# Kernel tuning notes

Measured on AMD Instinct MI355X. Metric: run time of the kernel, lower is better.

## Reference

```python
import jax, jax.numpy as jnp
import numpy as np

L, H, F_IN, OUT = 6, 2048, 2048, 2048
LN_EPS = 1e-5


def setup_inputs() -> dict:
    key = jax.random.key(0)
    ks = jax.random.split(key, 10)
    bound = 1.0 / np.sqrt(H)
    u = lambda k, shape: jax.random.uniform(k, shape, jnp.float32, -bound, bound)
    return {
        "x": jax.random.normal(ks[0], (1, 1, F_IN), jnp.float32),
        "hidden": jax.random.normal(ks[1], (L, 1, H), jnp.float32),
        "w_ih": u(ks[2], (L, 3 * H, H)),   # layer0 input size == H by construction
        "w_hh": u(ks[3], (L, 3 * H, H)),
        "b_ih": u(ks[4], (L, 3 * H)),
        "b_hh": u(ks[5], (L, 3 * H)),
        "ln_gamma": jnp.ones((H,), jnp.float32),
        "ln_beta": jnp.zeros((H,), jnp.float32),
        "lin_w": u(ks[6], (OUT, H)),
        "lin_b": u(ks[7], (OUT,)),
    }


def _gru_stack(x_t, hidden, w_ih, w_hh, b_ih, b_hh):
    # x_t: [B, H]; hidden: [L, B, H]. PyTorch gate order: r, z, n.
    def layer(inp, params):
        wi, wh, bi, bh, h = params
        gi = (inp @ wi.T + bi).reshape(inp.shape[0], 3, -1)  # [B,3,H]
        gh = (h @ wh.T + bh).reshape(h.shape[0], 3, -1)
        r = jax.nn.sigmoid(gi[:, 0] + gh[:, 0])
        z = jax.nn.sigmoid(gi[:, 1] + gh[:, 1])
        n = jnp.tanh(gi[:, 2] + r * gh[:, 2])
        h_new = (1.0 - z) * n + z * h
        return h_new, h_new

    top, new_hidden = jax.lax.scan(layer, x_t, (w_ih, w_hh, b_ih, b_hh, hidden))
    return top, new_hidden  # [B,H], [L,B,H]


def reference(x, hidden, w_ih, w_hh, b_ih, b_hh, ln_gamma, ln_beta, lin_w, lin_b):
    x_t = x[:, -1, :]  # [B, F_in]; T=1 so this is the only step
    out, new_hidden = _gru_stack(x_t, hidden, w_ih, w_hh, b_ih, b_hh)
    # LayerNorm over last dim
    mu = jnp.mean(out, axis=-1, keepdims=True)
    var = jnp.mean(jnp.square(out - mu), axis=-1, keepdims=True)
    out = (out - mu) * jax.lax.rsqrt(var + LN_EPS) * ln_gamma + ln_beta
    pred = out @ lin_w.T + lin_b + x_t[:, :OUT]
    return pred, new_hidden
```

## Files before the change

kernel.cpp:

```cpp
#include <hip/hip_runtime.h>


constexpr int HID = 2048;
constexpr int NL  = 6;
constexpr int G3  = 3 * HID;

__device__ __forceinline__ float wave_sum(float s){
  #pragma unroll
  for(int off = 32; off; off >>= 1) s += __shfl_down(s, off, 64);
  return s;
}

__device__ __forceinline__ float dot_f32(const float* __restrict__ row,
                                         const float* __restrict__ v, int lane){
  const float4* r4 = (const float4*)row;
  const float4* v4 = (const float4*)v;
  float s = 0.f;
  #pragma unroll
  for(int it = 0; it < 8; ++it){
    int idx = lane + 64 * it;
    float4 w = r4[idx], a = v4[idx];
    s += w.x * a.x + w.y * a.y + w.z * a.z + w.w * a.w;
  }
  return s;
}

__global__ __launch_bounds__(384) void k_layer(
    const float* __restrict__ w_ih_l,
    const float* __restrict__ w_hh_l,
    const float* __restrict__ b_ih_l,
    const float* __restrict__ b_hh_l,
    const float* __restrict__ h_l,
    const float* __restrict__ inp,
    float* __restrict__ h_new_ws,
    float* __restrict__ h_new_out)
{
  int j    = blockIdx.x;
  int wave = threadIdx.x >> 6;
  int lane = threadIdx.x & 63;
  __shared__ float sums[6];
  float s;
  if(wave < 3){
    s = dot_f32(w_ih_l + (size_t)(wave * HID + j) * HID, inp, lane);
  } else {
    s = dot_f32(w_hh_l + (size_t)((wave - 3) * HID + j) * HID, h_l, lane);
  }
  s = wave_sum(s);
  if(lane == 0) sums[wave] = s;
  __syncthreads();
  if(threadIdx.x == 0){
    float gi_r = sums[0] + b_ih_l[j];
    float gi_z = sums[1] + b_ih_l[HID + j];
    float gi_n = sums[2] + b_ih_l[2 * HID + j];
    float gh_r = sums[3] + b_hh_l[j];
    float gh_z = sums[4] + b_hh_l[HID + j];
    float gh_n = sums[5] + b_hh_l[2 * HID + j];
    float r = 1.f / (1.f + __expf(-(gi_r + gh_r)));
    float z = 1.f / (1.f + __expf(-(gi_z + gh_z)));
    float n = tanhf(gi_n + r * gh_n);
    float hn = (1.f - z) * n + z * h_l[j];
    h_new_ws[j]  = hn;
    h_new_out[j] = hn;
  }
}

__global__ __launch_bounds__(256) void k_layernorm(
    const float* __restrict__ h,
    const float* __restrict__ gamma,
    const float* __restrict__ beta,
    float* __restrict__ out)
{
  __shared__ float rs[4], rs2[4];
  __shared__ float s_mu, s_istd;
  int wave = threadIdx.x >> 6, lane = threadIdx.x & 63;
  float s = 0.f, s2 = 0.f;
  for(int i = threadIdx.x; i < HID; i += 256){ float v = h[i]; s += v; s2 += v * v; }
  #pragma unroll
  for(int off = 32; off; off >>= 1){ s += __shfl_down(s, off, 64); s2 += __shfl_down(s2, off, 64); }
  if(lane == 0){ rs[wave] = s; rs2[wave] = s2; }
  __syncthreads();
  if(threadIdx.x == 0){
    float S  = rs[0] + rs[1] + rs[2] + rs[3];
    float S2 = rs2[0] + rs2[1] + rs2[2] + rs2[3];
    float m   = S * (1.f / HID);
    float var = S2 * (1.f / HID) - m * m;
    s_mu = m; s_istd = rsqrtf(var + 1e-5f);
  }
  __syncthreads();
  float mu = s_mu, istd = s_istd;
  for(int i = threadIdx.x; i < HID; i += 256){
    out[i] = (h[i] - mu) * istd * gamma[i] + beta[i];
  }
}

__global__ __launch_bounds__(256) void k_linear(
    const float* __restrict__ v,
    const float* __restrict__ lin_w,
    const float* __restrict__ lin_b,
    const float* __restrict__ x,
    float* __restrict__ pred)
{
  int o    = blockIdx.x * 4 + (threadIdx.x >> 6);
  int lane = threadIdx.x & 63;
  float s = dot_f32(lin_w + (size_t)o * HID, v, lane);
  s = wave_sum(s);
  if(lane == 0) pred[o] = s + lin_b[o] + x[o];
}

extern "C" void kernel_launch(void* const* d_in, const int* in_sizes, int n_in,
                              void* d_out, int out_size, void* d_ws, size_t ws_size,
                              hipStream_t stream){
  const float* x      = (const float*)d_in[0];
  const float* hidden = (const float*)d_in[1];
  const float* w_ih   = (const float*)d_in[2];
  const float* w_hh   = (const float*)d_in[3];
  const float* b_ih   = (const float*)d_in[4];
  const float* b_hh   = (const float*)d_in[5];
  const float* gamma  = (const float*)d_in[6];
  const float* beta   = (const float*)d_in[7];
  const float* lin_w  = (const float*)d_in[8];
  const float* lin_b  = (const float*)d_in[9];
  float* out = (float*)d_out;

  float* buf = (float*)d_ws;

  for(int l = 0; l < NL; ++l){
    k_layer<<<HID, 384, 0, stream>>>(
        w_ih + (size_t)l * G3 * HID,
        w_hh + (size_t)l * G3 * HID,
        b_ih + (size_t)l * G3,
        b_hh + (size_t)l * G3,
        hidden + (size_t)l * HID,
        (l == 0) ? x : buf + (size_t)(l - 1) * HID,
        buf + (size_t)l * HID,
        out + HID + (size_t)l * HID);
  }
  k_layernorm<<<1, 256, 0, stream>>>(buf + 5 * HID, gamma, beta, buf + 6 * HID);
  k_linear<<<HID / 4, 256, 0, stream>>>(buf + 6 * HID, lin_w, lin_b, x, out);
}
```

Before: 604.3 us.

## Stream GRU and linear weight rows through LDS with double-buffered async loads

Rewrites the GRU layer and output linear kernels so each wave owns one output row and streams its six (or one) weight rows into LDS with global_load_lds in double-buffered halves, waiting on vmcnt manually. Input and hidden vectors are also staged once per block in LDS. The goal is to overlap weight fetches with dot-product math and cut redundant vector loads, in exchange for fewer waves in flight, heavy LDS use per block, and fragile hand-written waitcnt ordering.

```diff
diff --git a/kernel.cpp b/kernel.cpp
--- a/kernel.cpp
+++ b/kernel.cpp
@@ -11,21 +11,22 @@
   return s;
 }
 
-__device__ __forceinline__ float dot_f32(const float* __restrict__ row,
-                                         const float* __restrict__ v, int lane){
-  const float4* r4 = (const float4*)row;
-  const float4* v4 = (const float4*)v;
-  float s = 0.f;
-  #pragma unroll
-  for(int it = 0; it < 8; ++it){
-    int idx = lane + 64 * it;
-    float4 w = r4[idx], a = v4[idx];
-    s += w.x * a.x + w.y * a.y + w.z * a.z + w.w * a.w;
-  }
-  return s;
-}
-
-__global__ __launch_bounds__(384) void k_layer(
+__device__ __forceinline__ void gls16(const void* g, void* l){
+  __builtin_amdgcn_global_load_lds(
+      (const __attribute__((address_space(1))) void*)g,
+      (__attribute__((address_space(3))) void*)l,
+      16, 0, 0);
+}
+
+__device__ __forceinline__ void stage_half(float4* dst, const float* rowbase,
+                                           int hf, int lane){
+  const char* g = (const char*)rowbase + hf * 4096 + lane * 16;
+  char* l = (char*)dst;
+  #pragma unroll
+  for(int c = 0; c < 4; ++c) gls16(g + c * 1024, l + c * 1024);
+}
+
+__global__ __launch_bounds__(256) void k_layer(
     const float* __restrict__ w_ih_l,
     const float* __restrict__ w_hh_l,
     const float* __restrict__ b_ih_l,
@@ -35,26 +36,71 @@
     float* __restrict__ h_new_ws,
     float* __restrict__ h_new_out)
 {
-  int j    = blockIdx.x;
-  int wave = threadIdx.x >> 6;
-  int lane = threadIdx.x & 63;
-  __shared__ float sums[6];
-  float s;
-  if(wave < 3){
-    s = dot_f32(w_ih_l + (size_t)(wave * HID + j) * HID, inp, lane);
-  } else {
-    s = dot_f32(w_hh_l + (size_t)((wave - 3) * HID + j) * HID, h_l, lane);
-  }
-  s = wave_sum(s);
-  if(lane == 0) sums[wave] = s;
-  __syncthreads();
-  if(threadIdx.x == 0){
-    float gi_r = sums[0] + b_ih_l[j];
-    float gi_z = sums[1] + b_ih_l[HID + j];
-    float gi_n = sums[2] + b_ih_l[2 * HID + j];
-    float gh_r = sums[3] + b_hh_l[j];
-    float gh_z = sums[4] + b_hh_l[HID + j];
-    float gh_n = sums[5] + b_hh_l[2 * HID + j];
+  __shared__ float4 stg[4][2][256];
+  __shared__ float4 vvs[2][512];
+
+  const int wave = threadIdx.x >> 6;
+  const int lane = threadIdx.x & 63;
+  const int j    = blockIdx.x * 4 + wave;
+
+  const float* rp[6] = {
+    w_ih_l + (size_t)(0 * HID + j) * HID,
+    w_ih_l + (size_t)(1 * HID + j) * HID,
+    w_ih_l + (size_t)(2 * HID + j) * HID,
+    w_hh_l + (size_t)(0 * HID + j) * HID,
+    w_hh_l + (size_t)(1 * HID + j) * HID,
+    w_hh_l + (size_t)(2 * HID + j) * HID };
+
+  {
+    const int c0 = wave * 2;
+    gls16((const char*)inp + (c0    ) * 1024 + lane * 16, (char*)&vvs[0][0] + (c0    ) * 1024);
+    gls16((const char*)inp + (c0 + 1) * 1024 + lane * 16, (char*)&vvs[0][0] + (c0 + 1) * 1024);
+    gls16((const char*)h_l + (c0    ) * 1024 + lane * 16, (char*)&vvs[1][0] + (c0    ) * 1024);
+    gls16((const char*)h_l + (c0 + 1) * 1024 + lane * 16, (char*)&vvs[1][0] + (c0 + 1) * 1024);
+  }
+  stage_half(&stg[wave][0][0], rp[0], 0, lane);
+  stage_half(&stg[wave][1][0], rp[0], 1, lane);
+  asm volatile("s_waitcnt vmcnt(8)" ::: "memory");
+  __builtin_amdgcn_sched_barrier(0);
+  __syncthreads();
+
+  float acc[6] = {0.f, 0.f, 0.f, 0.f, 0.f, 0.f};
+  #pragma unroll
+  for(int k = 0; k < 12; ++k){
+    if(k < 11) { asm volatile("s_waitcnt vmcnt(4)" ::: "memory"); }
+    else       { asm volatile("s_waitcnt vmcnt(0)" ::: "memory"); }
+    __builtin_amdgcn_sched_barrier(0);
+    const float4* w = &stg[wave][k & 1][0];
+    const float4* v = ((k >> 1) < 3) ? &vvs[0][(k & 1) * 256]
+                                     : &vvs[1][(k & 1) * 256];
+    float s = 0.f;
+    #pragma unroll
+    for(int c = 0; c < 4; ++c){
+      float4 a = w[c * 64 + lane];
+      float4 b = v[c * 64 + lane];
+      s += a.x * b.x + a.y * b.y + a.z * b.z + a.w * b.w;
+    }
+    acc[k >> 1] += s;
+    if(k < 10){
+      asm volatile("s_waitcnt lgkmcnt(0)" ::: "memory");
+      stage_half(&stg[wave][k & 1][0], rp[(k + 2) >> 1], (k + 2) & 1, lane);
+    }
+  }
+
+  const float g0 = wave_sum(acc[0]);
+  const float g1 = wave_sum(acc[1]);
+  const float g2 = wave_sum(acc[2]);
+  const float g3 = wave_sum(acc[3]);
+  const float g4 = wave_sum(acc[4]);
+  const float g5 = wave_sum(acc[5]);
+
+  if(lane == 0){
+    float gi_r = g0 + b_ih_l[j];
+    float gi_z = g1 + b_ih_l[HID + j];
+    float gi_n = g2 + b_ih_l[2 * HID + j];
+    float gh_r = g3 + b_hh_l[j];
+    float gh_z = g4 + b_hh_l[HID + j];
+    float gh_n = g5 + b_hh_l[2 * HID + j];
     float r = 1.f / (1.f + __expf(-(gi_r + gh_r)));
     float z = 1.f / (1.f + __expf(-(gi_z + gh_z)));
     float n = tanhf(gi_n + r * gh_n);
@@ -100,11 +146,44 @@
     const float* __restrict__ x,
     float* __restrict__ pred)
 {
-  int o    = blockIdx.x * 4 + (threadIdx.x >> 6);
-  int lane = threadIdx.x & 63;
-  float s = dot_f32(lin_w + (size_t)o * HID, v, lane);
-  s = wave_sum(s);
-  if(lane == 0) pred[o] = s + lin_b[o] + x[o];
+  __shared__ float4 stg[4][2][256];
+  __shared__ float4 vbs[512];
+
+  const int wave = threadIdx.x >> 6;
+  const int lane = threadIdx.x & 63;
+  const int o    = blockIdx.x * 4 + wave;
+  const float* row = lin_w + (size_t)o * HID;
+
+  {
+    const int c0 = wave * 2;
+    gls16((const char*)v + (c0    ) * 1024 + lane * 16, (char*)&vbs[0] + (c0    ) * 1024);
+    gls16((const char*)v + (c0 + 1) * 1024 + lane * 16, (char*)&vbs[0] + (c0 + 1) * 1024);
+  }
+  stage_half(&stg[wave][0][0], row, 0, lane);
+  stage_half(&stg[wave][1][0], row, 1, lane);
+  asm volatile("s_waitcnt vmcnt(8)" ::: "memory");
+  __builtin_amdgcn_sched_barrier(0);
+  __syncthreads();
+
+  float acc = 0.f;
+  #pragma unroll
+  for(int k = 0; k < 2; ++k){
+    if(k == 0) { asm volatile("s_waitcnt vmcnt(4)" ::: "memory"); }
+    else       { asm volatile("s_waitcnt vmcnt(0)" ::: "memory"); }
+    __builtin_amdgcn_sched_barrier(0);
+    const float4* w = &stg[wave][k][0];
+    const float4* vb = &vbs[k * 256];
+    float s = 0.f;
+    #pragma unroll
+    for(int c = 0; c < 4; ++c){
+      float4 a = w[c * 64 + lane];
+      float4 b = vb[c * 64 + lane];
+      s += a.x * b.x + a.y * b.y + a.z * b.z + a.w * b.w;
+    }
+    acc += s;
+  }
+  acc = wave_sum(acc);
+  if(lane == 0) pred[o] = acc + lin_b[o] + x[o];
 }
 
 extern "C" void kernel_launch(void* const* d_in, const int* in_sizes, int n_in,
@@ -125,7 +204,7 @@
   float* buf = (float*)d_ws;
 
   for(int l = 0; l < NL; ++l){
-    k_layer<<<HID, 384, 0, stream>>>(
+    k_layer<<<HID / 4, 256, 0, stream>>>(
         w_ih + (size_t)l * G3 * HID,
         w_hh + (size_t)l * G3 * HID,
         b_ih + (size_t)l * G3,
```

Result: no change. 608.1 us (+0.6%).

## Fuse GRU layers, layernorm and linear into one persistent kernel with grid barriers

Applied to the files above, without the earlier changes.

Replaces eight kernel launches with one persistent kernel of 256 blocks that loops over the six GRU layers, separated by an atomic-counter grid barrier, then runs layernorm and the output linear in the same kernel. Each wave now computes all six gate dot products for one hidden unit, with the input and hidden vectors staged in shared memory and weights read through nontemporal loads. This removes per-launch overhead and the tail gaps between layers. In exchange it only uses 256 blocks to stream about 600 MB of weights, and it relies on all blocks being co-resident for the spin barrier.

```diff
diff --git a/kernel.cpp b/kernel.cpp
--- a/kernel.cpp
+++ b/kernel.cpp
@@ -1,9 +1,13 @@
 #include <hip/hip_runtime.h>
 
 
-constexpr int HID = 2048;
-constexpr int NL  = 6;
-constexpr int G3  = 3 * HID;
+constexpr int HID  = 2048;
+constexpr int NL   = 6;
+constexpr int G3   = 3 * HID;
+constexpr int NBLK = 256;
+constexpr int NTHR = 512;
+
+typedef float fx4 __attribute__((ext_vector_type(4)));
 
 __device__ __forceinline__ float wave_sum(float s){
   #pragma unroll
@@ -11,100 +15,154 @@
   return s;
 }
 
-__device__ __forceinline__ float dot_f32(const float* __restrict__ row,
-                                         const float* __restrict__ v, int lane){
-  const float4* r4 = (const float4*)row;
-  const float4* v4 = (const float4*)v;
-  float s = 0.f;
-  #pragma unroll
-  for(int it = 0; it < 8; ++it){
-    int idx = lane + 64 * it;
-    float4 w = r4[idx], a = v4[idx];
-    s += w.x * a.x + w.y * a.y + w.z * a.z + w.w * a.w;
-  }
-  return s;
+__device__ __forceinline__ fx4 ntl(const float* p){
+  return __builtin_nontemporal_load((const fx4*)p);
 }
 
-__global__ __launch_bounds__(384) void k_layer(
-    const float* __restrict__ w_ih_l,
-    const float* __restrict__ w_hh_l,
-    const float* __restrict__ b_ih_l,
-    const float* __restrict__ b_hh_l,
-    const float* __restrict__ h_l,
-    const float* __restrict__ inp,
-    float* __restrict__ h_new_ws,
-    float* __restrict__ h_new_out)
-{
-  int j    = blockIdx.x;
-  int wave = threadIdx.x >> 6;
-  int lane = threadIdx.x & 63;
-  __shared__ float sums[6];
-  float s;
-  if(wave < 3){
-    s = dot_f32(w_ih_l + (size_t)(wave * HID + j) * HID, inp, lane);
-  } else {
-    s = dot_f32(w_hh_l + (size_t)((wave - 3) * HID + j) * HID, h_l, lane);
-  }
-  s = wave_sum(s);
-  if(lane == 0) sums[wave] = s;
+__device__ __forceinline__ void gbar(unsigned* bar, unsigned target){
   __syncthreads();
   if(threadIdx.x == 0){
-    float gi_r = sums[0] + b_ih_l[j];
-    float gi_z = sums[1] + b_ih_l[HID + j];
-    float gi_n = sums[2] + b_ih_l[2 * HID + j];
-    float gh_r = sums[3] + b_hh_l[j];
-    float gh_z = sums[4] + b_hh_l[HID + j];
-    float gh_n = sums[5] + b_hh_l[2 * HID + j];
-    float r = 1.f / (1.f + __expf(-(gi_r + gh_r)));
-    float z = 1.f / (1.f + __expf(-(gi_z + gh_z)));
-    float n = tanhf(gi_n + r * gh_n);
-    float hn = (1.f - z) * n + z * h_l[j];
-    h_new_ws[j]  = hn;
-    h_new_out[j] = hn;
+    __threadfence();
+    __hip_atomic_fetch_add(bar, 1u, __ATOMIC_ACQ_REL, __HIP_MEMORY_SCOPE_AGENT);
+    while(__hip_atomic_load(bar, __ATOMIC_ACQUIRE, __HIP_MEMORY_SCOPE_AGENT) < target)
+      __builtin_amdgcn_s_sleep(2);
+    __threadfence();
   }
+  __syncthreads();
 }
 
-__global__ __launch_bounds__(256) void k_layernorm(
-    const float* __restrict__ h,
+__global__ void k_zero(unsigned* bar){ *bar = 0u; }
+
+__global__ __launch_bounds__(NTHR) void k_fused(
+    const float* __restrict__ x,
+    const float* __restrict__ hidden,
+    const float* __restrict__ w_ih,
+    const float* __restrict__ w_hh,
+    const float* __restrict__ b_ih,
+    const float* __restrict__ b_hh,
     const float* __restrict__ gamma,
     const float* __restrict__ beta,
-    float* __restrict__ out)
-{
-  __shared__ float rs[4], rs2[4];
-  __shared__ float s_mu, s_istd;
-  int wave = threadIdx.x >> 6, lane = threadIdx.x & 63;
-  float s = 0.f, s2 = 0.f;
-  for(int i = threadIdx.x; i < HID; i += 256){ float v = h[i]; s += v; s2 += v * v; }
-  #pragma unroll
-  for(int off = 32; off; off >>= 1){ s += __shfl_down(s, off, 64); s2 += __shfl_down(s2, off, 64); }
-  if(lane == 0){ rs[wave] = s; rs2[wave] = s2; }
-  __syncthreads();
-  if(threadIdx.x == 0){
-    float S  = rs[0] + rs[1] + rs[2] + rs[3];
-    float S2 = rs2[0] + rs2[1] + rs2[2] + rs2[3];
-    float m   = S * (1.f / HID);
-    float var = S2 * (1.f / HID) - m * m;
-    s_mu = m; s_istd = rsqrtf(var + 1e-5f);
-  }
-  __syncthreads();
-  float mu = s_mu, istd = s_istd;
-  for(int i = threadIdx.x; i < HID; i += 256){
-    out[i] = (h[i] - mu) * istd * gamma[i] + beta[i];
-  }
-}
-
-__global__ __launch_bounds__(256) void k_linear(
-    const float* __restrict__ v,
     const float* __restrict__ lin_w,
     const float* __restrict__ lin_b,
-    const float* __restrict__ x,
-    float* __restrict__ pred)
+    float* __restrict__ out,
+    float* __restrict__ buf,
+    unsigned* __restrict__ bar)
 {
-  int o    = blockIdx.x * 4 + (threadIdx.x >> 6);
-  int lane = threadIdx.x & 63;
-  float s = dot_f32(lin_w + (size_t)o * HID, v, lane);
-  s = wave_sum(s);
-  if(lane == 0) pred[o] = s + lin_b[o] + x[o];
+  __shared__ float vin[HID];
+  __shared__ float vh [HID];
+  __shared__ float red[8], red2[8];
+  __shared__ float s_mu, s_istd;
+
+  const int tid  = threadIdx.x;
+  const int wave = tid >> 6;
+  const int lane = tid & 63;
+  const int j    = blockIdx.x * 8 + wave;
+
+  for(int l = 0; l < NL; ++l){
+    const float* inp = (l == 0) ? x : buf + (size_t)(l - 1) * HID;
+    const float* hl  = hidden + (size_t)l * HID;
+
+    ((float4*)vin)[tid] = ((const float4*)inp)[tid];
+    ((float4*)vh )[tid] = ((const float4*)hl )[tid];
+    __syncthreads();
+
+    const float* wib = w_ih + (size_t)l * G3 * HID + (size_t)j * HID;
+    const float* whb = w_hh + (size_t)l * G3 * HID + (size_t)j * HID;
+    const float* R0 = wib;
+    const float* R1 = wib + (size_t)HID * HID;
+    const float* R2 = wib + (size_t)2 * HID * HID;
+    const float* R3 = whb;
+    const float* R4 = whb + (size_t)HID * HID;
+    const float* R5 = whb + (size_t)2 * HID * HID;
+    const float4* A  = (const float4*)vin;
+    const float4* Hh = (const float4*)vh;
+
+    float a0 = 0.f, a1 = 0.f, a2 = 0.f, a3 = 0.f, a4 = 0.f, a5 = 0.f;
+    #pragma unroll
+    for(int it = 0; it < 8; ++it){
+      const int idx = lane + 64 * it;
+      const float4 va = A[idx];
+      const float4 vb = Hh[idx];
+      const fx4 w0 = ntl(R0 + 4 * idx);
+      const fx4 w1 = ntl(R1 + 4 * idx);
+      const fx4 w2 = ntl(R2 + 4 * idx);
+      const fx4 w3 = ntl(R3 + 4 * idx);
+      const fx4 w4 = ntl(R4 + 4 * idx);
+      const fx4 w5 = ntl(R5 + 4 * idx);
+      a0 += w0.x*va.x + w0.y*va.y + w0.z*va.z + w0.w*va.w;
+      a1 += w1.x*va.x + w1.y*va.y + w1.z*va.z + w1.w*va.w;
+      a2 += w2.x*va.x + w2.y*va.y + w2.z*va.z + w2.w*va.w;
+      a3 += w3.x*vb.x + w3.y*vb.y + w3.z*vb.z + w3.w*vb.w;
+      a4 += w4.x*vb.x + w4.y*vb.y + w4.z*vb.z + w4.w*vb.w;
+      a5 += w5.x*vb.x + w5.y*vb.y + w5.z*vb.z + w5.w*vb.w;
+    }
+
+    const float g0 = wave_sum(a0);
+    const float g1 = wave_sum(a1);
+    const float g2 = wave_sum(a2);
+    const float g3 = wave_sum(a3);
+    const float g4 = wave_sum(a4);
+    const float g5 = wave_sum(a5);
+
+    if(lane == 0){
+      const float* bi = b_ih + (size_t)l * G3;
+      const float* bh = b_hh + (size_t)l * G3;
+      float gi_r = g0 + bi[j];
+      float gi_z = g1 + bi[HID + j];
+      float gi_n = g2 + bi[2 * HID + j];
+      float gh_r = g3 + bh[j];
+      float gh_z = g4 + bh[HID + j];
+      float gh_n = g5 + bh[2 * HID + j];
+      float r = 1.f / (1.f + __expf(-(gi_r + gh_r)));
+      float z = 1.f / (1.f + __expf(-(gi_z + gh_z)));
+      float n = tanhf(gi_n + r * gh_n);
+      float hn = (1.f - z) * n + z * vh[j];
+      buf[(size_t)l * HID + j] = hn;
+      out[HID + (size_t)l * HID + j] = hn;
+    }
+    gbar(bar, (unsigned)(NBLK * (l + 1)));
+  }
+
+  const float* htop = buf + (size_t)(NL - 1) * HID;
+  {
+    float s = 0.f, s2 = 0.f;
+    for(int i = tid; i < HID; i += NTHR){ float v = htop[i]; s += v; s2 += v * v; }
+    #pragma unroll
+    for(int off = 32; off; off >>= 1){
+      s  += __shfl_down(s,  off, 64);
+      s2 += __shfl_down(s2, off, 64);
+    }
+    if(lane == 0){ red[wave] = s; red2[wave] = s2; }
+    __syncthreads();
+    if(tid == 0){
+      float S = 0.f, S2 = 0.f;
+      #pragma unroll
+      for(int w = 0; w < 8; ++w){ S += red[w]; S2 += red2[w]; }
+      float m   = S * (1.f / HID);
+      float var = S2 * (1.f / HID) - m * m;
+      s_mu = m; s_istd = rsqrtf(var + 1e-5f);
+    }
+    __syncthreads();
+    const float mu = s_mu, istd = s_istd;
+    for(int i = tid; i < HID; i += NTHR)
+      vin[i] = (htop[i] - mu) * istd * gamma[i] + beta[i];
+    __syncthreads();
+  }
+
+  {
+    const float* R  = lin_w + (size_t)j * HID;
+    const float4* A = (const float4*)vin;
+    float s = 0.f;
+    #pragma unroll
+    for(int it = 0; it < 8; ++it){
+      const int idx = lane + 64 * it;
+      const fx4 w = ntl(R + 4 * idx);
+      const float4 a = A[idx];
+      s += w.x*a.x + w.y*a.y + w.z*a.z + w.w*a.w;
+    }
+    s = wave_sum(s);
+    if(lane == 0) out[j] = s + lin_b[j] + x[j];
+  }
 }
 
 extern "C" void kernel_launch(void* const* d_in, const int* in_sizes, int n_in,
@@ -121,20 +179,11 @@
   const float* lin_w  = (const float*)d_in[8];
   const float* lin_b  = (const float*)d_in[9];
   float* out = (float*)d_out;
+  float* buf = (float*)d_ws;
+  unsigned* bar = (unsigned*)((char*)d_ws + (size_t)NL * HID * 4);
 
-  float* buf = (float*)d_ws;
-
-  for(int l = 0; l < NL; ++l){
-    k_layer<<<HID, 384, 0, stream>>>(
-        w_ih + (size_t)l * G3 * HID,
-        w_hh + (size_t)l * G3 * HID,
-        b_ih + (size_t)l * G3,
-        b_hh + (size_t)l * G3,
-        hidden + (size_t)l * HID,
-        (l == 0) ? x : buf + (size_t)(l - 1) * HID,
-        buf + (size_t)l * HID,
-        out + HID + (size_t)l * HID);
-  }
-  k_layernorm<<<1, 256, 0, stream>>>(buf + 5 * HID, gamma, beta, buf + 6 * HID);
-  k_linear<<<HID / 4, 256, 0, stream>>>(buf + 6 * HID, lin_w, lin_b, x, out);
+  k_zero<<<1, 1, 0, stream>>>(bar);
+  k_fused<<<NBLK, NTHR, 0, stream>>>(
+      x, hidden, w_ih, w_hh, b_ih, b_hh, gamma, beta,
+      lin_w, lin_b, out, buf, bar);
 }
```

Result: slower. 692.7 us (+14.6%).
